# Kernel optimization log

Measured on AMD Instinct MI355X. Metric: run time of the kernel, lower is better.

The kernel has to match this reference:

```python
import jax, jax.numpy as jnp
import numpy as np

OUT_F, IN_F = 4096, 4096
WEIGHT_NUMEL = OUT_F * IN_F
NUM_CHUNKS, CHUNK_SIZE = 16384, 1024
D_ALPHA, HIDDEN = 64, 256
TOKENS = 256


def setup_inputs() -> dict:
    key = jax.random.key(0)
    ks = jax.random.split(key, 7)
    s = 0.05  # keep activations in a sane range
    return {
        "x": jax.random.normal(ks[0], (TOKENS, IN_F), jnp.float32),
        "codebook": jax.random.normal(ks[1], (NUM_CHUNKS, D_ALPHA), jnp.float32) * s,
        "w1": jax.random.normal(ks[2], (HIDDEN, D_ALPHA), jnp.float32) * s,
        "b1": jax.random.normal(ks[3], (HIDDEN,), jnp.float32) * s,
        "w2": jax.random.normal(ks[4], (CHUNK_SIZE, HIDDEN), jnp.float32) * s,
        "b2": jax.random.normal(ks[5], (CHUNK_SIZE,), jnp.float32) * s,
        "bias": jax.random.normal(ks[6], (OUT_F,), jnp.float32) * s,
    }


def reference(x, codebook, w1, b1, w2, b2, bias):
    # materialize_weight: alpha = codebook[start:start+num_chunks] (here: all rows)
    alpha = codebook[:NUM_CHUNKS]                                  # [num_chunks, d_alpha]
    # shared decoder psi: Linear -> GELU(exact) -> Linear (chunked loop == single GEMM)
    h = jax.nn.gelu(alpha @ w1.T + b1, approximate=False)          # [num_chunks, hidden]
    chunks = h @ w2.T + b2                                         # [num_chunks, chunk_size]
    w = chunks.reshape(-1)[:WEIGHT_NUMEL].reshape(OUT_F, IN_F)     # assemble weight
    # F.linear(x, w, b) = x @ w.T + b
    return x @ w.T + bias
```

## Files before the change

### kernel.cpp

```cpp
#include <hip/hip_runtime.h>
#include <math.h>

#define OUT_F      4096
#define IN_F       4096
#define NUM_CHUNKS 16384
#define CHUNK_SIZE 1024
#define D_ALPHA    64
#define HIDDEN     256
#define TOKENS     256

typedef __attribute__((ext_vector_type(8))) __bf16 bf16x8;
typedef __attribute__((ext_vector_type(4))) __bf16 bf16x4;
typedef __attribute__((ext_vector_type(4))) float f32x4;

__device__ __forceinline__ void gl2lds16(const void* g, void* l) {
    __builtin_amdgcn_global_load_lds(
        (const __attribute__((address_space(1))) void*)g,
        (__attribute__((address_space(3))) void*)l,
        16, 0, 0);
}

__global__ __launch_bounds__(256) void prep_kernel(
    const float* __restrict__ cb, const float* __restrict__ w1,
    const float* __restrict__ b1, const float* __restrict__ x,
    const float* __restrict__ b2, const float* __restrict__ w2,
    __bf16* __restrict__ H, __bf16* __restrict__ xb,
    float* __restrict__ xb2, __bf16* __restrict__ w2t) {
    __shared__ char smem[16384];
    const int b   = blockIdx.x;
    const int tid = threadIdx.x;

    if (b < 1024) {
        const int by = b >> 2;
        const int bx = b & 3;
        const int c0 = by * 64, h0 = bx * 64;
        __bf16* sA = (__bf16*)smem;
        __bf16* sB = (__bf16*)(smem + 8192);
        const float4* cb4 = reinterpret_cast<const float4*>(cb) + (size_t)by * 1024;
        const float4* w14 = reinterpret_cast<const float4*>(w1) + (size_t)bx * 1024;
#pragma unroll
        for (int q = 0; q < 4; ++q) {
            const int idx = q * 256 + tid;
            float4 va = cb4[idx];
            float4 vb = w14[idx];
            bf16x4 oa, ob;
            oa.x = (__bf16)va.x; oa.y = (__bf16)va.y; oa.z = (__bf16)va.z; oa.w = (__bf16)va.w;
            ob.x = (__bf16)vb.x; ob.y = (__bf16)vb.y; ob.z = (__bf16)vb.z; ob.w = (__bf16)vb.w;
            *reinterpret_cast<bf16x4*>(sA + idx * 4) = oa;
            *reinterpret_cast<bf16x4*>(sB + idx * 4) = ob;
        }
        __syncthreads();
        const int wave = tid >> 6, lane = tid & 63;
        const int wm = (wave & 1) * 32, wn = (wave >> 1) * 32;
        const int fr = lane & 15, fq = lane >> 4;
        f32x4 acc[2][2] = {};
        bf16x8 af[2][2], bv[2][2];
#pragma unroll
        for (int i = 0; i < 2; ++i)
#pragma unroll
            for (int u = 0; u < 2; ++u) {
                af[i][u] = *reinterpret_cast<const bf16x8*>(
                    sA + (wm + i * 16 + fr) * 64 + u * 32 + fq * 8);
                bv[i][u] = *reinterpret_cast<const bf16x8*>(
                    sB + (wn + i * 16 + fr) * 64 + u * 32 + fq * 8);
            }
#pragma unroll
        for (int u = 0; u < 2; ++u)
#pragma unroll
            for (int i = 0; i < 2; ++i)
#pragma unroll
                for (int j = 0; j < 2; ++j)
                    acc[i][j] = __builtin_amdgcn_mfma_f32_16x16x32_bf16(
                        af[i][u], bv[j][u], acc[i][j], 0, 0, 0);
#pragma unroll
        for (int j = 0; j < 2; ++j) {
            const int col = h0 + wn + j * 16 + fr;
            const float bb = b1[col];
#pragma unroll
            for (int i = 0; i < 2; ++i) {
                const int rbase = c0 + wm + i * 16 + fq * 4;
#pragma unroll
                for (int r = 0; r < 4; ++r) {
                    float v = acc[i][j][r] + bb;
                    float g = 0.5f * v * (1.0f + erff(v * 0.70710678118654752f));
                    H[(size_t)(rbase + r) * 256 + col] = (__bf16)g;
                }
            }
        }
    } else if (b < 1280) {
        float* ws_ = (float*)smem;
        const int t = b - 1024;
        const float4* xr  = reinterpret_cast<const float4*>(x + (size_t)t * IN_F);
        const float4* b24 = reinterpret_cast<const float4*>(b2);
        bf16x4* xb4 = reinterpret_cast<bf16x4*>(xb + (size_t)t * IN_F);
        float acc = 0.0f;
#pragma unroll
        for (int ii = 0; ii < 4; ++ii) {
            const int idx = ii * 256 + tid;
            float4 v = xr[idx];
            bf16x4 o;
            o.x = (__bf16)v.x; o.y = (__bf16)v.y; o.z = (__bf16)v.z; o.w = (__bf16)v.w;
            xb4[idx] = o;
            float4 bb = b24[idx & 255];
            acc += v.x * bb.x + v.y * bb.y + v.z * bb.z + v.w * bb.w;
        }
#pragma unroll
        for (int off = 32; off > 0; off >>= 1) acc += __shfl_down(acc, off, 64);
        if ((tid & 63) == 0) ws_[tid >> 6] = acc;
        __syncthreads();
        if (tid == 0) xb2[t] = ws_[0] + ws_[1] + ws_[2] + ws_[3];
    } else {
        float (*tile)[33] = (float (*)[33])smem;
        const int bb = b - 1280;
        const int h0 = (bb & 7) * 32;
        const int p0 = (bb >> 3) * 32;
        const int r = tid >> 5;
        const int c = tid & 31;
#pragma unroll
        for (int ii = 0; ii < 4; ++ii)
            tile[r + 8 * ii][c] = w2[(size_t)(p0 + r + 8 * ii) * HIDDEN + h0 + c];
        __syncthreads();
#pragma unroll
        for (int ii = 0; ii < 4; ++ii)
            w2t[(size_t)(h0 + r + 8 * ii) * CHUNK_SIZE + p0 + c] =
                (__bf16)tile[c][r + 8 * ii];
    }
}

template <int BK, int EPI>
__global__ __launch_bounds__(256) void gemm_bt64(
    const __bf16* __restrict__ A, const __bf16* __restrict__ B,
    const float* __restrict__ bias, const float* __restrict__ rowterm,
    void* __restrict__ Cv, int M, int N, int K) {
    __shared__ __bf16 sA[64 * BK];
    __shared__ __bf16 sB[64 * BK];
    const int tid = threadIdx.x;
    const int m0 = blockIdx.y * 64;
    const int n0 = blockIdx.x * 64;

    constexpr int NC = BK / 32;
    int rowc[NC], colc[NC];
#pragma unroll
    for (int c = 0; c < NC; ++c) {
        const int flat = c * 2048 + tid * 8;
        rowc[c] = flat / BK;
        colc[c] = flat % BK;
    }

    const int wave = tid >> 6, lane = tid & 63;
    const int wm = (wave & 1) * 32, wn = (wave >> 1) * 32;
    const int fr = lane & 15, fq = lane >> 4;

    f32x4 acc[2][2] = {};

    for (int k0 = 0; k0 < K; k0 += BK) {
#pragma unroll
        for (int c = 0; c < NC; ++c) {
            gl2lds16(A + (size_t)(m0 + rowc[c]) * K + k0 + colc[c],
                     sA + c * 2048 + tid * 8);
            gl2lds16(B + (size_t)(n0 + rowc[c]) * K + k0 + colc[c],
                     sB + c * 2048 + tid * 8);
        }
        __syncthreads();

#pragma unroll
        for (int u = 0; u < BK / 32; ++u) {
            bf16x8 af[2], bv[2];
#pragma unroll
            for (int i = 0; i < 2; ++i) {
                af[i] = *reinterpret_cast<const bf16x8*>(
                    sA + (wm + i * 16 + fr) * BK + u * 32 + fq * 8);
                bv[i] = *reinterpret_cast<const bf16x8*>(
                    sB + (wn + i * 16 + fr) * BK + u * 32 + fq * 8);
            }
#pragma unroll
            for (int i = 0; i < 2; ++i)
#pragma unroll
                for (int j = 0; j < 2; ++j)
                    acc[i][j] = __builtin_amdgcn_mfma_f32_16x16x32_bf16(
                        af[i], bv[j], acc[i][j], 0, 0, 0);
        }
        __syncthreads();
    }

    if (EPI == 0) {
        __bf16* C = (__bf16*)Cv;
#pragma unroll
        for (int j = 0; j < 2; ++j) {
            const int col = n0 + wn + j * 16 + fr;
#pragma unroll
            for (int i = 0; i < 2; ++i) {
                const int rbase = m0 + wm + i * 16 + fq * 4;
#pragma unroll
                for (int r = 0; r < 4; ++r)
                    C[(size_t)(rbase + r) * N + col] = (__bf16)acc[i][j][r];
            }
        }
    } else {
        float* C = (float*)Cv;
#pragma unroll
        for (int j = 0; j < 2; ++j) {
            const int col = n0 + wn + j * 16 + fr;
            const float bvs = bias[col];
#pragma unroll
            for (int i = 0; i < 2; ++i) {
                const int rbase = m0 + wm + i * 16 + fq * 4;
#pragma unroll
                for (int r = 0; r < 4; ++r)
                    C[(size_t)(rbase + r) * N + col] =
                        acc[i][j][r] + bvs + rowterm[rbase + r];
            }
        }
    }
}

extern "C" void kernel_launch(void* const* d_in, const int* in_sizes, int n_in,
                              void* d_out, int out_size, void* d_ws, size_t ws_size,
                              hipStream_t stream) {
    const float* x        = (const float*)d_in[0];
    const float* codebook = (const float*)d_in[1];
    const float* w1       = (const float*)d_in[2];
    const float* b1       = (const float*)d_in[3];
    const float* w2       = (const float*)d_in[4];
    const float* b2       = (const float*)d_in[5];
    const float* bias     = (const float*)d_in[6];
    float* out = (float*)d_out;

    char* ws = (char*)d_ws;
    __bf16* xb  = (__bf16*)(ws);
    __bf16* w2t = (__bf16*)(ws + (2u << 20));
    __bf16* H   = (__bf16*)(ws + (3u << 20));
    __bf16* Y   = (__bf16*)(ws + (11u << 20));
    float*  xb2 = (float*)(ws + (12u << 20));

    prep_kernel<<<1536, 256, 0, stream>>>(codebook, w1, b1, x, b2, w2,
                                          H, xb, xb2, w2t);

    {
        dim3 grid(HIDDEN / 64, 1024 / 64, 1);
        gemm_bt64<128, 0><<<grid, 256, 0, stream>>>(
            xb, w2t, nullptr, nullptr, Y, 1024, HIDDEN, 1024);
    }

    {
        dim3 grid(OUT_F / 64, TOKENS / 64, 1);
        gemm_bt64<128, 1><<<grid, 256, 0, stream>>>(
            Y, H, bias, xb2, out, TOKENS, OUT_F, 1024);
    }
}
```

Before: 105.9 us.

## Fuse x·w2 GEMM into prep kernel, converting and transposing on the fly

The separate x-to-bf16 conversion, w2 transpose and the first small GEMM are merged into the prep kernel. 64 extra blocks compute Y = x·w2 directly from fp32 inputs, converting to bf16 and transposing w2 while staging into shared memory with a padded stride. This removes one kernel launch and the round trips through the intermediate xb and w2t buffers. In exchange those 64 GEMM blocks do slower, non-async loads, run alongside the H blocks, and raise shared memory per block to about 33KB for all branches, which may reduce occupancy.

```diff
diff --git a/kernel.cpp b/kernel.cpp
--- a/kernel.cpp
+++ b/kernel.cpp
@@ -20,19 +20,94 @@
         16, 0, 0);
 }
 
-__global__ __launch_bounds__(256) void prep_kernel(
+__global__ __launch_bounds__(256) void fused_prep(
     const float* __restrict__ cb, const float* __restrict__ w1,
     const float* __restrict__ b1, const float* __restrict__ x,
     const float* __restrict__ b2, const float* __restrict__ w2,
-    __bf16* __restrict__ H, __bf16* __restrict__ xb,
-    float* __restrict__ xb2, __bf16* __restrict__ w2t) {
-    __shared__ char smem[16384];
+    __bf16* __restrict__ H, __bf16* __restrict__ Y,
+    float* __restrict__ xb2) {
+    __shared__ __align__(16) char smem[33792];
     const int b   = blockIdx.x;
     const int tid = threadIdx.x;
 
-    if (b < 1024) {
-        const int by = b >> 2;
-        const int bx = b & 3;
+    if (b < 64) {
+        constexpr int BK = 128, SBS = 136;
+        const int mt = b & 15, nt = b >> 4;
+        const int m0 = mt * 64, h0 = nt * 64;
+        __bf16* sA = (__bf16*)smem;
+        __bf16* sB = (__bf16*)(smem + 16384);
+
+        const int wave = tid >> 6, lane = tid & 63;
+        const int wm = (wave & 1) * 32, wn = (wave >> 1) * 32;
+        const int fr = lane & 15, fq = lane >> 4;
+        f32x4 acc[2][2] = {};
+
+        for (int k0 = 0; k0 < 1024; k0 += BK) {
+#pragma unroll
+            for (int c = 0; c < 8; ++c) {
+                const int idx = c * 256 + tid;
+                const int row = idx >> 5, k4 = idx & 31;
+                float4 v = *reinterpret_cast<const float4*>(
+                    x + (size_t)(m0 + row) * 1024 + k0 + k4 * 4);
+                bf16x4 o;
+                o.x = (__bf16)v.x; o.y = (__bf16)v.y;
+                o.z = (__bf16)v.z; o.w = (__bf16)v.w;
+                *reinterpret_cast<bf16x4*>(sA + row * BK + k4 * 4) = o;
+            }
+#pragma unroll
+            for (int c = 0; c < 2; ++c) {
+                const int idx = c * 256 + tid;
+                const int h4 = idx & 15, pq = idx >> 4;
+                float4 vv[4];
+#pragma unroll
+                for (int dp = 0; dp < 4; ++dp)
+                    vv[dp] = *reinterpret_cast<const float4*>(
+                        w2 + (size_t)(k0 + pq * 4 + dp) * HIDDEN + h0 + h4 * 4);
+#pragma unroll
+                for (int dh = 0; dh < 4; ++dh) {
+                    bf16x4 o;
+                    o.x = (__bf16)((const float*)&vv[0])[dh];
+                    o.y = (__bf16)((const float*)&vv[1])[dh];
+                    o.z = (__bf16)((const float*)&vv[2])[dh];
+                    o.w = (__bf16)((const float*)&vv[3])[dh];
+                    *reinterpret_cast<bf16x4*>(
+                        sB + (h4 * 4 + dh) * SBS + pq * 4) = o;
+                }
+            }
+            __syncthreads();
+#pragma unroll
+            for (int u = 0; u < BK / 32; ++u) {
+                bf16x8 af[2], bv[2];
+#pragma unroll
+                for (int i = 0; i < 2; ++i) {
+                    af[i] = *reinterpret_cast<const bf16x8*>(
+                        sA + (wm + i * 16 + fr) * BK + u * 32 + fq * 8);
+                    bv[i] = *reinterpret_cast<const bf16x8*>(
+                        sB + (wn + i * 16 + fr) * SBS + u * 32 + fq * 8);
+                }
+#pragma unroll
+                for (int i = 0; i < 2; ++i)
+#pragma unroll
+                    for (int j = 0; j < 2; ++j)
+                        acc[i][j] = __builtin_amdgcn_mfma_f32_16x16x32_bf16(
+                            af[i], bv[j], acc[i][j], 0, 0, 0);
+            }
+            __syncthreads();
+        }
+#pragma unroll
+        for (int j = 0; j < 2; ++j) {
+            const int col = h0 + wn + j * 16 + fr;
+#pragma unroll
+            for (int i = 0; i < 2; ++i) {
+                const int rbase = m0 + wm + i * 16 + fq * 4;
+#pragma unroll
+                for (int r = 0; r < 4; ++r)
+                    Y[(size_t)(rbase + r) * HIDDEN + col] = (__bf16)acc[i][j][r];
+            }
+        }
+    } else if (b < 1088) {
+        const int bb = b - 64;
+        const int by = bb >> 2, bx = bb & 3;
         const int c0 = by * 64, h0 = bx * 64;
         __bf16* sA = (__bf16*)smem;
         __bf16* sB = (__bf16*)(smem + 8192);
@@ -75,32 +150,28 @@
 #pragma unroll
         for (int j = 0; j < 2; ++j) {
             const int col = h0 + wn + j * 16 + fr;
-            const float bb = b1[col];
+            const float bb1 = b1[col];
 #pragma unroll
             for (int i = 0; i < 2; ++i) {
                 const int rbase = c0 + wm + i * 16 + fq * 4;
 #pragma unroll
                 for (int r = 0; r < 4; ++r) {
-                    float v = acc[i][j][r] + bb;
+                    float v = acc[i][j][r] + bb1;
                     float g = 0.5f * v * (1.0f + erff(v * 0.70710678118654752f));
                     H[(size_t)(rbase + r) * 256 + col] = (__bf16)g;
                 }
             }
         }
-    } else if (b < 1280) {
+    } else {
         float* ws_ = (float*)smem;
-        const int t = b - 1024;
+        const int t = b - 1088;
         const float4* xr  = reinterpret_cast<const float4*>(x + (size_t)t * IN_F);
         const float4* b24 = reinterpret_cast<const float4*>(b2);
-        bf16x4* xb4 = reinterpret_cast<bf16x4*>(xb + (size_t)t * IN_F);
         float acc = 0.0f;
 #pragma unroll
         for (int ii = 0; ii < 4; ++ii) {
             const int idx = ii * 256 + tid;
             float4 v = xr[idx];
-            bf16x4 o;
-            o.x = (__bf16)v.x; o.y = (__bf16)v.y; o.z = (__bf16)v.z; o.w = (__bf16)v.w;
-            xb4[idx] = o;
             float4 bb = b24[idx & 255];
             acc += v.x * bb.x + v.y * bb.y + v.z * bb.z + v.w * bb.w;
         }
@@ -109,29 +180,14 @@
         if ((tid & 63) == 0) ws_[tid >> 6] = acc;
         __syncthreads();
         if (tid == 0) xb2[t] = ws_[0] + ws_[1] + ws_[2] + ws_[3];
-    } else {
-        float (*tile)[33] = (float (*)[33])smem;
-        const int bb = b - 1280;
-        const int h0 = (bb & 7) * 32;
-        const int p0 = (bb >> 3) * 32;
-        const int r = tid >> 5;
-        const int c = tid & 31;
-#pragma unroll
-        for (int ii = 0; ii < 4; ++ii)
-            tile[r + 8 * ii][c] = w2[(size_t)(p0 + r + 8 * ii) * HIDDEN + h0 + c];
-        __syncthreads();
-#pragma unroll
-        for (int ii = 0; ii < 4; ++ii)
-            w2t[(size_t)(h0 + r + 8 * ii) * CHUNK_SIZE + p0 + c] =
-                (__bf16)tile[c][r + 8 * ii];
-    }
-}
-
-template <int BK, int EPI>
-__global__ __launch_bounds__(256) void gemm_bt64(
+    }
+}
+
+__global__ __launch_bounds__(256) void gemm_out(
     const __bf16* __restrict__ A, const __bf16* __restrict__ B,
     const float* __restrict__ bias, const float* __restrict__ rowterm,
-    void* __restrict__ Cv, int M, int N, int K) {
+    float* __restrict__ C, int M, int N, int K) {
+    constexpr int BK = 128;
     __shared__ __bf16 sA[64 * BK];
     __shared__ __bf16 sB[64 * BK];
     const int tid = threadIdx.x;
@@ -183,33 +239,17 @@
         __syncthreads();
     }
 
-    if (EPI == 0) {
-        __bf16* C = (__bf16*)Cv;
-#pragma unroll
-        for (int j = 0; j < 2; ++j) {
-            const int col = n0 + wn + j * 16 + fr;
-#pragma unroll
-            for (int i = 0; i < 2; ++i) {
-                const int rbase = m0 + wm + i * 16 + fq * 4;
-#pragma unroll
-                for (int r = 0; r < 4; ++r)
-                    C[(size_t)(rbase + r) * N + col] = (__bf16)acc[i][j][r];
-            }
-        }
-    } else {
-        float* C = (float*)Cv;
-#pragma unroll
-        for (int j = 0; j < 2; ++j) {
-            const int col = n0 + wn + j * 16 + fr;
-            const float bvs = bias[col];
-#pragma unroll
-            for (int i = 0; i < 2; ++i) {
-                const int rbase = m0 + wm + i * 16 + fq * 4;
-#pragma unroll
-                for (int r = 0; r < 4; ++r)
-                    C[(size_t)(rbase + r) * N + col] =
-                        acc[i][j][r] + bvs + rowterm[rbase + r];
-            }
+#pragma unroll
+    for (int j = 0; j < 2; ++j) {
+        const int col = n0 + wn + j * 16 + fr;
+        const float bvs = bias[col];
+#pragma unroll
+        for (int i = 0; i < 2; ++i) {
+            const int rbase = m0 + wm + i * 16 + fq * 4;
+#pragma unroll
+            for (int r = 0; r < 4; ++r)
+                C[(size_t)(rbase + r) * N + col] =
+                    acc[i][j][r] + bvs + rowterm[rbase + r];
         }
     }
 }
@@ -227,24 +267,16 @@
     float* out = (float*)d_out;
 
     char* ws = (char*)d_ws;
-    __bf16* xb  = (__bf16*)(ws);
-    __bf16* w2t = (__bf16*)(ws + (2u << 20));
-    __bf16* H   = (__bf16*)(ws + (3u << 20));
-    __bf16* Y   = (__bf16*)(ws + (11u << 20));
-    float*  xb2 = (float*)(ws + (12u << 20));
-
-    prep_kernel<<<1536, 256, 0, stream>>>(codebook, w1, b1, x, b2, w2,
-                                          H, xb, xb2, w2t);
-
-    {
-        dim3 grid(HIDDEN / 64, 1024 / 64, 1);
-        gemm_bt64<128, 0><<<grid, 256, 0, stream>>>(
-            xb, w2t, nullptr, nullptr, Y, 1024, HIDDEN, 1024);
-    }
+    __bf16* H   = (__bf16*)(ws);
+    __bf16* Y   = (__bf16*)(ws + (8u << 20));
+    float*  xb2 = (float*)(ws + (9u << 20));
+
+    fused_prep<<<1344, 256, 0, stream>>>(codebook, w1, b1, x, b2, w2,
+                                         H, Y, xb2);
 
     {
         dim3 grid(OUT_F / 64, TOKENS / 64, 1);
-        gemm_bt64<128, 1><<<grid, 256, 0, stream>>>(
+        gemm_out<<<grid, 256, 0, stream>>>(
             Y, H, bias, xb2, out, TOKENS, OUT_F, 1024);
     }
 }
```

Measured after the change: 117.6 us. 11.1% more time.
